# Kernel optimization log

Measured on AMD Instinct MI355X. Metric: run time of the kernel, lower is better.

The kernel has to match this reference:

```python
import jax, jax.numpy as jnp
import numpy as np

KH, KW = 4, 4
N, P, IN_CH, OUT_CH = 50000, 32, 64, 64


def setup_inputs() -> dict:
    key = jax.random.key(0)
    k1, k2, k3, k4 = jax.random.split(key, 4)
    features = jax.random.normal(k1, (N, IN_CH), jnp.float32)
    receivers = jax.random.randint(k2, (N, P), 0, N)
    # relative offsets scaled so most neighbors fall inside the support radius
    relative_positions = jax.random.normal(k3, (N, P, 2), jnp.float32) * 0.35
    window_support = jnp.float32(1.0)
    a = 3  # window exponent (1 - d^2/R^2)^a
    kernel = jax.random.uniform(k4, (KH, KW, IN_CH, OUT_CH), jnp.float32, -0.05, 0.05)
    bias = jnp.zeros((OUT_CH,), jnp.float32)
    return {"features": features, "receivers": receivers,
            "relative_positions": relative_positions,
            "window_support": window_support, "a": a,
            "kernel": kernel, "bias": bias}


def reference(features, receivers, relative_positions, window_support, a, kernel, bias):
    kh, kw, in_ch, out_ch = kernel.shape
    n, p = receivers.shape
    g_bins = kh * kw

    gathered = features[receivers]                      # [N,P,in] gather
    r = relative_positions / window_support             # normalized to [-1,1]
    d2 = jnp.sum(r * r, axis=-1)                        # [N,P]
    win = jnp.maximum(1.0 - d2, 0.0) ** a               # radial window

    # map normalized position to continuous kernel-grid coordinates
    gy = jnp.clip((r[..., 0] + 1.0) * 0.5 * (kh - 1), 0.0, kh - 1)
    gx = jnp.clip((r[..., 1] + 1.0) * 0.5 * (kw - 1), 0.0, kw - 1)
    y0 = jnp.clip(jnp.floor(gy).astype(jnp.int32), 0, kh - 2)
    x0 = jnp.clip(jnp.floor(gx).astype(jnp.int32), 0, kw - 2)
    fy = gy - y0
    fx = gx - x0

    # accumulate window*bilinear-weighted features into kernel bins per output point,
    # avoiding materializing a per-edge [in,out] interpolated filter
    n_idx = jnp.arange(n)[:, None]                      # broadcasts over P
    M = jnp.zeros((n, g_bins, in_ch), features.dtype)
    corners = [(0, 0, (1 - fy) * (1 - fx)), (0, 1, (1 - fy) * fx),
               (1, 0, fy * (1 - fx)), (1, 1, fy * fx)]
    for dy, dx, bw in corners:
        g = (y0 + dy) * kw + (x0 + dx)                  # [N,P] flat bin index
        M = M.at[n_idx, g].add((bw * win)[..., None] * gathered)

    out = jnp.einsum('ngi,gio->no', M, kernel.reshape(g_bins, in_ch, out_ch))
    return out / p + bias
```

## Files before the change

### kernel.cpp

```cpp
#include <hip/hip_runtime.h>
#include <hip/hip_bf16.h>

typedef unsigned short u16;
typedef unsigned int u32;

#define THREADS 512
constexpr int CH = 64;
constexpr int PP = 32;
constexpr int TM = 16;

constexpr int W_OFF  = 0;
constexpr int RB_OFF = 0;
constexpr int MB_OFF = 16384;
constexpr int LDS_BYTES = 49152;

typedef __attribute__((ext_vector_type(8))) short short8;
typedef __attribute__((ext_vector_type(4))) float f32x4;

static __device__ __forceinline__ u16 f2bf_rne(float f) {
  __hip_bfloat16 h = __float2bfloat16(f);
  return __builtin_bit_cast(u16, h);
}
static __device__ __forceinline__ u16 rbf(float f) {
  u32 u = __builtin_bit_cast(u32, f);
  return (u16)((u + 0x8000u) >> 16);
}

__global__ void prep_feat(const float* __restrict__ in, u16* __restrict__ outb, int n2) {
  int i = blockIdx.x * blockDim.x + threadIdx.x;
  if (i < n2) {
    float2 v = ((const float2*)in)[i];
    u32 u = (u32)f2bf_rne(v.x) | ((u32)f2bf_rne(v.y) << 16);
    ((u32*)outb)[i] = u;
  }
}

__global__ void prep_k2f(const float* __restrict__ kern, u16* __restrict__ k2f) {
  int d = blockIdx.x * blockDim.x + threadIdx.x;
  int e = d & 7, l = (d >> 3) & 63, ot = (d >> 9) & 3, ks = d >> 11;
  int k = ks * 32 + (l >> 4) * 8 + e;
  int o = ot * 16 + (l & 15);
  k2f[d] = f2bf_rne(kern[k * 64 + o]);
}

__global__ __launch_bounds__(THREADS, 6) void cconv_main(
    const int* __restrict__ recv, const float* __restrict__ relpos,
    const float* __restrict__ wsup, const int* __restrict__ aptr,
    const u16* __restrict__ fbf, const u16* __restrict__ k2f,
    const float* __restrict__ bias, float* __restrict__ out) {
  __shared__ __align__(16) char smem[LDS_BYTES];
  const int tid = threadIdx.x;
  const int n0 = blockIdx.x * TM;
  const int wid = tid >> 6, lane = tid & 63;
  const int l15 = lane & 15, l4 = lane >> 4;
  const int pairp = wid & 3;
  const int half  = wid >> 2;

  {
    const float invws = 1.0f / wsup[0];
    int a = aptr[0];
    if (a < 0 || a > 64) a = (int)(*(const float*)aptr);
    const int e = tid;
    const int m = e >> 5, p = e & 31;
    const int ei = (n0 + m) * PP + p;
    const float2 rp2 = ((const float2*)relpos)[ei];
    const float rx = rp2.x * invws, ry = rp2.y * invws;
    const float d2 = rx * rx + ry * ry;
    const float w1 = fmaxf(1.0f - d2, 0.0f);
    float win = 1.0f;
    for (int q = 0; q < a; ++q) win *= w1;
    float gy = fminf(fmaxf((rx + 1.0f) * 1.5f, 0.0f), 3.0f);
    float gx = fminf(fmaxf((ry + 1.0f) * 1.5f, 0.0f), 3.0f);
    int y0 = (int)gy; y0 = y0 > 2 ? 2 : y0;
    int x0 = (int)gx; x0 = x0 > 2 ? 2 : x0;
    const float fy = gy - (float)y0, fx = gx - (float)x0;
    u16* wp = (u16*)(smem + W_OFF) + m * 512 + p;
    #pragma unroll
    for (int g = 0; g < 16; ++g) {
      const int y = g >> 2, x = g & 3;
      const float wyv = (y == y0) ? (1.0f - fy) : (y == y0 + 1) ? fy : 0.0f;
      const float wxv = (x == x0) ? (1.0f - fx) : (x == x0 + 1) ? fx : 0.0f;
      wp[g * 32] = rbf(win * wyv * wxv);
    }
  }
  __syncthreads();

  #pragma unroll
  for (int t = 0; t < 2; ++t) {
    const int m = wid * 2 + t;
    const int* rp = recv + (n0 + m) * PP + l4 * 8;
    const int4 A4 = *(const int4*)rp;
    const int4 B4 = *(const int4*)(rp + 4);
    const short8 af = *(const short8*)(smem + W_OFF + m * 1024 + l15 * 64 + l4 * 16);
    u32 vo[8];
    vo[0] = (u32)A4.x * 64u + (u32)l15; vo[1] = (u32)A4.y * 64u + (u32)l15;
    vo[2] = (u32)A4.z * 64u + (u32)l15; vo[3] = (u32)A4.w * 64u + (u32)l15;
    vo[4] = (u32)B4.x * 64u + (u32)l15; vo[5] = (u32)B4.y * 64u + (u32)l15;
    vo[6] = (u32)B4.z * 64u + (u32)l15; vo[7] = (u32)B4.w * 64u + (u32)l15;
    f32x4 accm[4];
    #pragma unroll
    for (int ib = 0; ib < 4; ++ib) {
      u32 q[8];
      #pragma unroll
      for (int e = 0; e < 8; ++e) q[e] = (u32)fbf[vo[e] + ib * 16];
      union { u32 u[4]; short8 s; } bb;
      #pragma unroll
      for (int j = 0; j < 4; ++j) bb.u[j] = q[2 * j] | (q[2 * j + 1] << 16);
      const f32x4 cz = {0.f, 0.f, 0.f, 0.f};
      accm[ib] = __builtin_amdgcn_mfma_f32_16x16x32_bf16(af, bb.s, cz, 0, 0, 0);
    }
    #pragma unroll
    for (int ib = 0; ib < 4; ++ib)
      #pragma unroll
      for (int r = 0; r < 4; ++r) {
        const int g = l4 * 4 + r;
        const u32 k = (u32)(g * 64 + ib * 16 + l15);
        u32 byt = (u32)m * 2048u + k * 2u;
        byt ^= ((u32)((m & 7) ^ (g & 7)) << 4);
        *(u16*)(smem + MB_OFF + byt) = rbf(accm[ib][r]);
      }
  }
  __syncthreads();

  f32x4 acc = {0.f, 0.f, 0.f, 0.f};
  {
    const u32 rowb = (u32)l15 * 2048u;
    const u32 swl = (u32)(l15 & 7) << 4;
    #pragma unroll 8
    for (int j = 0; j < 16; ++j) {
      const int ks = half * 16 + j;
      const u32 kc = (u32)ks * 32u + (u32)l4 * 8u;
      const u32 g7 = (((kc >> 6) & 7u) << 4);
      const u32 byt = (rowb + kc * 2u) ^ swl ^ g7;
      const short8 a2 = *(const short8*)(smem + MB_OFF + byt);
      const short8 b2 = *(const short8*)(k2f + ((u32)(ks * 4 + pairp) * 64u + (u32)lane) * 8u);
      acc = __builtin_amdgcn_mfma_f32_16x16x32_bf16(a2, b2, acc, 0, 0, 0);
    }
  }

  if (half == 1) {
    #pragma unroll
    for (int r = 0; r < 4; ++r) {
      const int row = l4 * 4 + r;
      const u32 byt = (u32)pairp * 1024u + (u32)row * 64u + (u32)((l15 ^ l4) * 4);
      *(float*)(smem + RB_OFF + byt) = acc[r];
    }
  }
  __syncthreads();
  if (half == 0) {
    #pragma unroll
    for (int r = 0; r < 4; ++r) {
      const int row = l4 * 4 + r;
      const u32 byt = (u32)pairp * 1024u + (u32)row * 64u + (u32)((l15 ^ l4) * 4);
      acc[r] += *(const float*)(smem + RB_OFF + byt);
    }
    const int o = pairp * 16 + l15;
    const float bv = bias[o];
    #pragma unroll
    for (int r = 0; r < 4; ++r)
      out[(n0 + l4 * 4 + r) * CH + o] = acc[r] * (1.0f / 32.0f) + bv;
  }
}

extern "C" void kernel_launch(void* const* d_in, const int* in_sizes, int n_in,
                              void* d_out, int out_size, void* d_ws, size_t ws_size,
                              hipStream_t stream) {
  const float* features = (const float*)d_in[0];
  const int* receivers  = (const int*)d_in[1];
  const float* relpos   = (const float*)d_in[2];
  const float* wsup     = (const float*)d_in[3];
  const int* aptr       = (const int*)d_in[4];
  const float* kern     = (const float*)d_in[5];
  const float* bias     = (const float*)d_in[6];
  float* out = (float*)d_out;

  const int N = in_sizes[0] / CH;
  u16* fbf = (u16*)d_ws;
  u16* k2f = (u16*)((char*)d_ws + (size_t)N * CH * 2);

  const int nfeat2 = in_sizes[0] / 2;
  prep_feat<<<dim3((nfeat2 + 255) / 256), dim3(256), 0, stream>>>(features, fbf, nfeat2);
  prep_k2f<<<dim3(65536 / 256), dim3(256), 0, stream>>>(kern, k2f);

  cconv_main<<<dim3(N / TM), dim3(THREADS), 0, stream>>>(
      receivers, relpos, wsup, aptr, fbf, k2f, bias, out);
}
```

Before: 54.96 us.

## Interleave bf16 feature layout for 8-byte gathers and fuse prep kernels

The bf16 feature copy is stored interleaved so that the four channels each lane needs (l15, l15+16, l15+32, l15+48) sit in one 8-byte word. Each neighbor then costs one uint2 load per lane instead of four separate 2-byte loads, and the MFMA B operands are assembled with shift/mask ops. The two prep kernels are merged into one launch to save launch overhead. The prep kernel's reads are now strided with poorer coalescing, and the extra packing ALU work is the cost of the change.

```diff
diff --git a/kernel.cpp b/kernel.cpp
--- a/kernel.cpp
+++ b/kernel.cpp
@@ -26,21 +26,28 @@
   return (u16)((u + 0x8000u) >> 16);
 }
 
-__global__ void prep_feat(const float* __restrict__ in, u16* __restrict__ outb, int n2) {
+__global__ void prep_all(const float* __restrict__ feat, u16* __restrict__ fbf,
+                         const float* __restrict__ kern, u16* __restrict__ k2f,
+                         int nq) {
   int i = blockIdx.x * blockDim.x + threadIdx.x;
-  if (i < n2) {
-    float2 v = ((const float2*)in)[i];
-    u32 u = (u32)f2bf_rne(v.x) | ((u32)f2bf_rne(v.y) << 16);
-    ((u32*)outb)[i] = u;
-  }
-}
-
-__global__ void prep_k2f(const float* __restrict__ kern, u16* __restrict__ k2f) {
-  int d = blockIdx.x * blockDim.x + threadIdx.x;
-  int e = d & 7, l = (d >> 3) & 63, ot = (d >> 9) & 3, ks = d >> 11;
-  int k = ks * 32 + (l >> 4) * 8 + e;
-  int o = ot * 16 + (l & 15);
-  k2f[d] = f2bf_rne(kern[k * 64 + o]);
+  if (i < nq) {
+    const int row = i >> 4, l15 = i & 15;
+    const float* src = feat + (size_t)row * 64 + l15;
+    const u32 a0 = f2bf_rne(src[0]);
+    const u32 a1 = f2bf_rne(src[16]);
+    const u32 a2 = f2bf_rne(src[32]);
+    const u32 a3 = f2bf_rne(src[48]);
+    uint2 w; w.x = a0 | (a1 << 16); w.y = a2 | (a3 << 16);
+    ((uint2*)fbf)[i] = w;
+  } else {
+    const int d = i - nq;
+    if (d < 65536) {
+      const int e = d & 7, l = (d >> 3) & 63, ot = (d >> 9) & 3, ks = d >> 11;
+      const int k = ks * 32 + (l >> 4) * 8 + e;
+      const int o = ot * 16 + (l & 15);
+      k2f[d] = f2bf_rne(kern[k * 64 + o]);
+    }
+  }
 }
 
 __global__ __launch_bounds__(THREADS, 6) void cconv_main(
@@ -55,6 +62,7 @@
   const int l15 = lane & 15, l4 = lane >> 4;
   const int pairp = wid & 3;
   const int half  = wid >> 2;
+  const char* fb2 = (const char*)fbf;
 
   {
     const float invws = 1.0f / wsup[0];
@@ -92,23 +100,30 @@
     const int4 A4 = *(const int4*)rp;
     const int4 B4 = *(const int4*)(rp + 4);
     const short8 af = *(const short8*)(smem + W_OFF + m * 1024 + l15 * 64 + l4 * 16);
-    u32 vo[8];
-    vo[0] = (u32)A4.x * 64u + (u32)l15; vo[1] = (u32)A4.y * 64u + (u32)l15;
-    vo[2] = (u32)A4.z * 64u + (u32)l15; vo[3] = (u32)A4.w * 64u + (u32)l15;
-    vo[4] = (u32)B4.x * 64u + (u32)l15; vo[5] = (u32)B4.y * 64u + (u32)l15;
-    vo[6] = (u32)B4.z * 64u + (u32)l15; vo[7] = (u32)B4.w * 64u + (u32)l15;
+    const int rv[8] = {A4.x, A4.y, A4.z, A4.w, B4.x, B4.y, B4.z, B4.w};
+    uint2 q2[8];
+    #pragma unroll
+    for (int e = 0; e < 8; ++e)
+      q2[e] = *(const uint2*)(fb2 + (size_t)(u32)rv[e] * 128u + (u32)l15 * 8u);
     f32x4 accm[4];
-    #pragma unroll
-    for (int ib = 0; ib < 4; ++ib) {
-      u32 q[8];
-      #pragma unroll
-      for (int e = 0; e < 8; ++e) q[e] = (u32)fbf[vo[e] + ib * 16];
-      union { u32 u[4]; short8 s; } bb;
-      #pragma unroll
-      for (int j = 0; j < 4; ++j) bb.u[j] = q[2 * j] | (q[2 * j + 1] << 16);
-      const f32x4 cz = {0.f, 0.f, 0.f, 0.f};
-      accm[ib] = __builtin_amdgcn_mfma_f32_16x16x32_bf16(af, bb.s, cz, 0, 0, 0);
-    }
+    const f32x4 cz = {0.f, 0.f, 0.f, 0.f};
+    union { u32 u[4]; short8 s; } bb;
+    #pragma unroll
+    for (int j = 0; j < 4; ++j)
+      bb.u[j] = (q2[2 * j].x & 0xffffu) | (q2[2 * j + 1].x << 16);
+    accm[0] = __builtin_amdgcn_mfma_f32_16x16x32_bf16(af, bb.s, cz, 0, 0, 0);
+    #pragma unroll
+    for (int j = 0; j < 4; ++j)
+      bb.u[j] = (q2[2 * j].x >> 16) | (q2[2 * j + 1].x & 0xffff0000u);
+    accm[1] = __builtin_amdgcn_mfma_f32_16x16x32_bf16(af, bb.s, cz, 0, 0, 0);
+    #pragma unroll
+    for (int j = 0; j < 4; ++j)
+      bb.u[j] = (q2[2 * j].y & 0xffffu) | (q2[2 * j + 1].y << 16);
+    accm[2] = __builtin_amdgcn_mfma_f32_16x16x32_bf16(af, bb.s, cz, 0, 0, 0);
+    #pragma unroll
+    for (int j = 0; j < 4; ++j)
+      bb.u[j] = (q2[2 * j].y >> 16) | (q2[2 * j + 1].y & 0xffff0000u);
+    accm[3] = __builtin_amdgcn_mfma_f32_16x16x32_bf16(af, bb.s, cz, 0, 0, 0);
     #pragma unroll
     for (int ib = 0; ib < 4; ++ib)
       #pragma unroll
@@ -178,9 +193,10 @@
   u16* fbf = (u16*)d_ws;
   u16* k2f = (u16*)((char*)d_ws + (size_t)N * CH * 2);
 
-  const int nfeat2 = in_sizes[0] / 2;
-  prep_feat<<<dim3((nfeat2 + 255) / 256), dim3(256), 0, stream>>>(features, fbf, nfeat2);
-  prep_k2f<<<dim3(65536 / 256), dim3(256), 0, stream>>>(kern, k2f);
+  const int nq = N * 16;
+  const int prep_total = nq + 65536;
+  prep_all<<<dim3((prep_total + 255) / 256), dim3(256), 0, stream>>>(
+      features, fbf, kern, k2f, nq);
 
   cconv_main<<<dim3(N / TM), dim3(THREADS), 0, stream>>>(
       receivers, relpos, wsup, aptr, fbf, k2f, bias, out);
```

Result: faster. 50.82 us (-7.5%).
